# Kernel tuning notes

Hardware: AMD Instinct MI355X
Metric: run time of the kernel (lower is better)

The kernel has to match this reference:

```python
import jax, jax.numpy as jnp
import numpy as np
from jax import lax

T, B = 256, 4096
H = 64  # lstm hidden/input size


def setup_inputs() -> dict:
    key = jax.random.key(0)
    ks = jax.random.split(key, 20)
    s = 0.1
    return {
        "x": jax.random.normal(ks[0], (T * B, 9), jnp.float32),
        "done": jax.random.randint(ks[1], (T * B,), 0, 2).astype(jnp.int32),
        "h0": jax.random.normal(ks[2], (1, B, H), jnp.float32),
        "c0": jax.random.normal(ks[3], (1, B, H), jnp.float32),
        # root MLP: Linear(9,32) ReLU Linear(32,64) ReLU (stored [in,out])
        "Wr1": jax.random.normal(ks[4], (9, 32), jnp.float32) * s,
        "br1": jnp.zeros((32,), jnp.float32),
        "Wr2": jax.random.normal(ks[5], (32, H), jnp.float32) * s,
        "br2": jnp.zeros((H,), jnp.float32),
        # LSTM(64,64): gate order i,f,g,o; stored [in, 4H]
        "Wih": jax.random.normal(ks[6], (H, 4 * H), jnp.float32) * s,
        "Whh": jax.random.normal(ks[7], (H, 4 * H), jnp.float32) * s,
        "b_lstm": jnp.zeros((4 * H,), jnp.float32),  # bias_ih + bias_hh (both init 0)
        # critic: Linear(64,16) Tanh Linear(16,8) Tanh Linear(8,1)
        "Wc1": jax.random.normal(ks[8], (H, 16), jnp.float32) * s,
        "bc1": jnp.zeros((16,), jnp.float32),
        "Wc2": jax.random.normal(ks[9], (16, 8), jnp.float32) * s,
        "bc2": jnp.zeros((8,), jnp.float32),
        "Wc3": jax.random.normal(ks[10], (8, 1), jnp.float32) * s,
        "bc3": jnp.zeros((1,), jnp.float32),
    }


def reference(x, done, h0, c0, Wr1, br1, Wr2, br2, Wih, Whh, b_lstm,
              Wc1, bc1, Wc2, bc2, Wc3, bc3):
    b = h0.shape[1]
    # root MLP on all T*B rows at once
    hidden = jax.nn.relu(jax.nn.relu(x @ Wr1 + br1) @ Wr2 + br2)  # [T*B, 64]
    t = hidden.shape[0] // b
    hid = hidden.reshape(t, b, H)
    d = done.reshape(t, b).astype(hidden.dtype)
    # precompute input projection for all timesteps (hoisted out of the scan)
    xp = hid @ Wih + b_lstm  # [T, B, 4H]

    def step(carry, inp):
        h, c = carry
        xpt, dt = inp
        m = (1.0 - dt)[:, None]  # reset state where episode is done
        h = h * m
        c = c * m
        g = xpt + h @ Whh  # [B, 4H]
        gi, gf, gg, go = jnp.split(g, 4, axis=-1)
        c = jax.nn.sigmoid(gf) * c + jax.nn.sigmoid(gi) * jnp.tanh(gg)
        h = jax.nn.sigmoid(go) * jnp.tanh(c)
        return (h, c), h

    (_, _), hs = lax.scan(step, (h0[0], c0[0]), (xp, d))
    new_hidden = hs.reshape(t * b, H)  # flatten like torch.cat + flatten(0,1)
    # critic head (get_value)
    v = jnp.tanh(new_hidden @ Wc1 + bc1)
    v = jnp.tanh(v @ Wc2 + bc2)
    return v @ Wc3 + bc3  # [T*B, 1]
```

## Files before the change

kernel.cpp:

```cpp
#include <hip/hip_runtime.h>
#include <hip/hip_bf16.h>


#define TT 256
#define BB 4096
#define TBROWS (TT * BB)
#define LOG2E 1.44269504088896340736f

typedef short bf16x8 __attribute__((ext_vector_type(8)));
typedef float f32x4 __attribute__((ext_vector_type(4)));

__device__ __forceinline__ unsigned bfbits(float x) {
  unsigned u = __float_as_uint(x);
  return (u + 0x7fffu + ((u >> 16) & 1u)) >> 16;
}
__device__ __forceinline__ unsigned pkbf(float lo, float hi) {
  return bfbits(lo) | (bfbits(hi) << 16);
}
__device__ __forceinline__ float rcpf_(float x) { return __builtin_amdgcn_rcpf(x); }
__device__ __forceinline__ float exp2f_(float x) { return __builtin_amdgcn_exp2f(x); }

#define BAR_LDS()                                                   \
  do {                                                              \
    asm volatile("s_waitcnt lgkmcnt(0)" ::: "memory");              \
    __builtin_amdgcn_s_barrier();                                   \
    asm volatile("" ::: "memory");                                  \
  } while (0)

__global__ __launch_bounds__(256) void k1m(const float* __restrict__ x,
                                           const float* __restrict__ Wr1,
                                           const float* __restrict__ br1,
                                           const float* __restrict__ Wr2,
                                           const float* __restrict__ br2,
                                           unsigned short* __restrict__ hb) {
  __shared__ int sBr1[2 * 256];
  __shared__ int sBr2[4 * 256];
  __shared__ float sx[4][208];
  __shared__ int h1s[4][324];

  const int tid = threadIdx.x;
  const int lane = tid & 63, wid = tid >> 6;
  const int g4 = lane >> 4, l15 = lane & 15;

  for (int i = tid; i < 512; i += 256) {
    int nt = i >> 8, rem = i & 255;
    int L = rem >> 2, d = rem & 3;
    int u = nt * 16 + (L & 15);
    int k0 = (L >> 4) * 4 + d;
    float v0 = (k0 < 9) ? Wr1[k0 * 32 + u] : 0.f;
    sBr1[i] = (int)bfbits(v0);
  }
  for (int i = tid; i < 1024; i += 256) {
    int nt = i >> 8, rem = i & 255;
    int L = rem >> 2, d = rem & 3;
    int u = nt * 16 + (L & 15);
    int p = (L >> 4) * 4 + d;
    sBr2[i] = (int)pkbf(Wr2[p * 64 + u], Wr2[(p + 16) * 64 + u]);
  }
  __syncthreads();

  float br1v[2] = {br1[l15], br1[16 + l15]};
  float br2v[4];
#pragma unroll
  for (int nt = 0; nt < 4; ++nt) br2v[nt] = br2[nt * 16 + l15];

  long gw = (long)blockIdx.x * 4 + wid;
  long nw = (long)gridDim.x * 4;
  for (long row0 = gw * 16; row0 < TBROWS; row0 += nw * 16) {
    {
      int j = lane;
      float v = x[row0 * 9 + j];
      int r = (j * 456) >> 12; int cc = j - r * 9;
      sx[wid][r * 12 + cc] = v;
      j = lane + 64;
      v = x[row0 * 9 + j];
      r = (j * 456) >> 12; cc = j - r * 9;
      sx[wid][r * 12 + cc] = v;
      if (lane < 16) {
        j = lane + 128;
        v = x[row0 * 9 + j];
        r = (j * 456) >> 12; cc = j - r * 9;
        sx[wid][r * 12 + cc] = v;
      }
    }
    float4 xq = *(const float4*)&sx[wid][l15 * 12 + g4 * 4];
    union { unsigned u[4]; bf16x8 v; } A1;
#pragma unroll
    for (int d = 0; d < 4; ++d) {
      float v = ((const float*)&xq)[d];
      v = (g4 * 4 + d < 9) ? v : 0.f;
      A1.u[d] = bfbits(v);
    }
    f32x4 c1[2];
#pragma unroll
    for (int nt = 0; nt < 2; ++nt) {
      c1[nt] = (f32x4){br1v[nt], br1v[nt], br1v[nt], br1v[nt]};
      c1[nt] = __builtin_amdgcn_mfma_f32_16x16x32_bf16(
          A1.v, *(const bf16x8*)&sBr1[nt * 256 + lane * 4], c1[nt], 0, 0, 0);
    }
#pragma unroll
    for (int r = 0; r < 4; ++r)
      h1s[wid][(g4 * 4 + r) * 20 + l15] =
          (int)pkbf(fmaxf(c1[0][r], 0.f), fmaxf(c1[1][r], 0.f));
    bf16x8 A2 = *(const bf16x8*)&h1s[wid][l15 * 20 + g4 * 4];
    f32x4 c2[4];
#pragma unroll
    for (int nt = 0; nt < 4; ++nt) {
      c2[nt] = (f32x4){br2v[nt], br2v[nt], br2v[nt], br2v[nt]};
      c2[nt] = __builtin_amdgcn_mfma_f32_16x16x32_bf16(
          A2, *(const bf16x8*)&sBr2[nt * 256 + lane * 4], c2[nt], 0, 0, 0);
    }
#pragma unroll
    for (int nt = 0; nt < 4; ++nt)
#pragma unroll
      for (int r = 0; r < 4; ++r)
        hb[(row0 + g4 * 4 + r) * 64 + nt * 16 + l15] =
            (unsigned short)bfbits(fmaxf(c2[nt][r], 0.f));
  }
}

__global__ __launch_bounds__(320) void k2m(
    const unsigned short* __restrict__ hb, const int* __restrict__ done,
    const float* __restrict__ h0, const float* __restrict__ c0,
    const float* __restrict__ Wih, const float* __restrict__ Whh,
    const float* __restrict__ bl,
    const float* __restrict__ Wc1, const float* __restrict__ bc1,
    const float* __restrict__ Wc2, const float* __restrict__ bc2,
    const float* __restrict__ Wc3, const float* __restrict__ bc3,
    float* __restrict__ out) {
  __shared__ __align__(16) unsigned short hT2[2][16 * 72];
  __shared__ float sv1[16 * 20];
  __shared__ int sdone[TT * 16];

  const int tid = threadIdx.x;
  const int lane = tid & 63;
  const int wid = tid >> 6;
  const int g4 = lane >> 4, l15 = lane & 15;
  const int base_b = blockIdx.x * 16;

  for (int i = tid; i < TT * 16; i += 320)
    sdone[i] = done[(long)(i >> 4) * BB + base_b + (i & 15)];

  union frag { unsigned u[4]; bf16x8 v; };
  frag Bih[4][2], Bhh[4][2];
  frag Bc1[2];
  float wc2a[16], wc2b[16];
  float c[4], bias_g[4];
  float bc1s = 0.f, bc2s0 = 0.f, bc2s1 = 0.f, wc3a = 0.f, wc3b = 0.f, bc3r = 0.f;

  if (wid < 4) {
#pragma unroll
    for (int g = 0; g < 4; ++g) {
      int nt = g * 4 + wid;
      int col = nt * 16 + l15;
      float sc = (g == 2) ? 2.f * LOG2E : LOG2E;
#pragma unroll
      for (int q = 0; q < 2; ++q)
#pragma unroll
        for (int d = 0; d < 4; ++d) {
          int k0 = q * 32 + g4 * 8 + 2 * d;
          Bih[g][q].u[d] = pkbf(Wih[k0 * 256 + col] * sc, Wih[(k0 + 1) * 256 + col] * sc);
          Bhh[g][q].u[d] = pkbf(Whh[k0 * 256 + col] * sc, Whh[(k0 + 1) * 256 + col] * sc);
        }
      bias_g[g] = bl[nt * 16 + l15] * sc;
    }
#pragma unroll
    for (int r = 0; r < 4; ++r) {
      int row = base_b + g4 * 4 + r;
      float m0 = 1.f - (float)done[row];
      c[r] = c0[row * 64 + wid * 16 + l15] * m0;
      hT2[1][(g4 * 4 + r) * 72 + wid * 16 + l15] =
          (unsigned short)bfbits(h0[row * 64 + wid * 16 + l15]);
    }
  } else {
    float S = 2.f * LOG2E;
#pragma unroll
    for (int q = 0; q < 2; ++q)
#pragma unroll
      for (int d = 0; d < 4; ++d) {
        int k0 = q * 32 + g4 * 8 + 2 * d;
        Bc1[q].u[d] = pkbf(Wc1[k0 * 16 + l15] * S, Wc1[(k0 + 1) * 16 + l15] * S);
      }
#pragma unroll
    for (int k = 0; k < 16; ++k) {
      wc2a[k] = Wc2[k * 8 + g4 * 2] * S;
      wc2b[k] = Wc2[k * 8 + g4 * 2 + 1] * S;
    }
    bc1s = bc1[l15] * S;
    bc2s0 = bc2[g4 * 2] * S;
    bc2s1 = bc2[g4 * 2 + 1] * S;
    wc3a = Wc3[g4 * 2];
    wc3b = Wc3[g4 * 2 + 1];
    bc3r = bc3[0];
  }
  __syncthreads();

  bf16x8 aA0 = {}, aA1 = {}, aB0 = {}, aB1 = {};
  int dnA = 0, dnB = 0;
  if (wid < 4) {
    long r0a = ((long)0 * BB + base_b + l15) * 64;
    long r1a = ((long)1 * BB + base_b + l15) * 64;
    aA0 = *(const bf16x8*)(hb + r0a + g4 * 8);
    aA1 = *(const bf16x8*)(hb + r0a + 32 + g4 * 8);
    aB0 = *(const bf16x8*)(hb + r1a + g4 * 8);
    aB1 = *(const bf16x8*)(hb + r1a + 32 + g4 * 8);
    dnA = sdone[0 * 16 + l15];
    dnB = sdone[1 * 16 + l15];
  }

  auto gate_step = [&](int t, bf16x8& x0, bf16x8& x1, int& dnv) {
    const unsigned short* rb = hT2[(t + 1) & 1];
    unsigned short* wb = hT2[t & 1];
    int4 r0 = *(const int4*)(rb + l15 * 72 + g4 * 8);
    int4 r1 = *(const int4*)(rb + l15 * 72 + 32 + g4 * 8);
    if (dnv != 0) { r0 = make_int4(0, 0, 0, 0); r1 = make_int4(0, 0, 0, 0); }
    union { int4 i4; bf16x8 v; } ah0, ah1;
    ah0.i4 = r0; ah1.i4 = r1;

    f32x4 accP[4], accQ[4];
#pragma unroll
    for (int g = 0; g < 4; ++g) {
      accP[g] = (f32x4){bias_g[g], bias_g[g], bias_g[g], bias_g[g]};
      accQ[g] = (f32x4){0.f, 0.f, 0.f, 0.f};
    }
#pragma unroll
    for (int g = 0; g < 4; ++g) {
      accP[g] = __builtin_amdgcn_mfma_f32_16x16x32_bf16(ah0.v, Bhh[g][0].v, accP[g], 0, 0, 0);
      accQ[g] = __builtin_amdgcn_mfma_f32_16x16x32_bf16(ah1.v, Bhh[g][1].v, accQ[g], 0, 0, 0);
    }
#pragma unroll
    for (int g = 0; g < 4; ++g) {
      accP[g] = __builtin_amdgcn_mfma_f32_16x16x32_bf16(x0, Bih[g][0].v, accP[g], 0, 0, 0);
      accQ[g] = __builtin_amdgcn_mfma_f32_16x16x32_bf16(x1, Bih[g][1].v, accQ[g], 0, 0, 0);
    }
    if (t + 2 < TT) {
      long nb = ((long)(t + 2) * BB + base_b + l15) * 64;
      x0 = *(const bf16x8*)(hb + nb + g4 * 8);
      x1 = *(const bf16x8*)(hb + nb + 32 + g4 * 8);
      dnv = sdone[(t + 2) * 16 + l15];
    }

    float out_h[4];
#pragma unroll
    for (int r = 0; r < 4; ++r) {
      float xi = accP[0][r] + accQ[0][r];
      float xf = accP[1][r] + accQ[1][r];
      float xg = accP[2][r] + accQ[2][r];
      float xo = accP[3][r] + accQ[3][r];
      float si = rcpf_(1.f + exp2f_(-xi));
      float sf = rcpf_(1.f + exp2f_(-xf));
      float so = rcpf_(1.f + exp2f_(-xo));
      float tg = fmaf(2.f, rcpf_(1.f + exp2f_(-xg)), -1.f);
      float cc = fmaf(sf, c[r], si * tg);
      float tc = fmaf(2.f, rcpf_(1.f + exp2f_(cc * (-2.f * LOG2E))), -1.f);
      out_h[r] = so * tc;
      float mn = (t + 1 < TT) ? (1.f - (float)sdone[(t + 1) * 16 + g4 * 4 + r]) : 1.f;
      c[r] = cc * mn;
    }
#pragma unroll
    for (int r = 0; r < 4; ++r)
      wb[(g4 * 4 + r) * 72 + wid * 16 + l15] = (unsigned short)bfbits(out_h[r]);
  };

  auto critic_step = [&](int tprev, const unsigned short* rb) {
    bf16x8 ca0 = *(const bf16x8*)(rb + l15 * 72 + g4 * 8);
    bf16x8 ca1 = *(const bf16x8*)(rb + l15 * 72 + 32 + g4 * 8);
    f32x4 a1 = (f32x4){bc1s, bc1s, bc1s, bc1s};
    a1 = __builtin_amdgcn_mfma_f32_16x16x32_bf16(ca0, Bc1[0].v, a1, 0, 0, 0);
    a1 = __builtin_amdgcn_mfma_f32_16x16x32_bf16(ca1, Bc1[1].v, a1, 0, 0, 0);
#pragma unroll
    for (int r = 0; r < 4; ++r) {
      float v1 = fmaf(2.f, rcpf_(1.f + exp2f_(-a1[r])), -1.f);
      sv1[(g4 * 4 + r) * 20 + l15] = v1;
    }
    float a2a = bc2s0, a2b = bc2s1;
    const float* vrow = &sv1[l15 * 20];
#pragma unroll
    for (int k = 0; k < 16; ++k) {
      float vk = vrow[k];
      a2a = fmaf(vk, wc2a[k], a2a);
      a2b = fmaf(vk, wc2b[k], a2b);
    }
    float v2a = fmaf(2.f, rcpf_(1.f + exp2f_(-a2a)), -1.f);
    float v2b = fmaf(2.f, rcpf_(1.f + exp2f_(-a2b)), -1.f);
    float p = fmaf(v2a, wc3a, v2b * wc3b);
    p += __shfl_xor(p, 16);
    p += __shfl_xor(p, 32);
    if (g4 == 0) out[(long)tprev * BB + base_b + l15] = p + bc3r;
  };

  for (int t2 = 0; t2 < TT; t2 += 2) {
    if (wid < 4) {
      gate_step(t2, aA0, aA1, dnA);
    } else {
      if (t2 > 0) critic_step(t2 - 1, hT2[(t2 + 1) & 1]);
    }
    BAR_LDS();
    if (wid < 4) {
      gate_step(t2 + 1, aB0, aB1, dnB);
    } else {
      critic_step(t2, hT2[(t2 + 2) & 1]);
    }
    BAR_LDS();
  }
  if (wid == 4) critic_step(TT - 1, hT2[(TT - 1) & 1]);
}

extern "C" void kernel_launch(void* const* d_in, const int* in_sizes, int n_in,
                              void* d_out, int out_size, void* d_ws, size_t ws_size,
                              hipStream_t stream) {
  const float* x = (const float*)d_in[0];
  const int* done = (const int*)d_in[1];
  const float* h0 = (const float*)d_in[2];
  const float* c0 = (const float*)d_in[3];
  const float* Wr1 = (const float*)d_in[4];
  const float* br1 = (const float*)d_in[5];
  const float* Wr2 = (const float*)d_in[6];
  const float* br2 = (const float*)d_in[7];
  const float* Wih = (const float*)d_in[8];
  const float* Whh = (const float*)d_in[9];
  const float* bl = (const float*)d_in[10];
  const float* Wc1 = (const float*)d_in[11];
  const float* bc1 = (const float*)d_in[12];
  const float* Wc2 = (const float*)d_in[13];
  const float* bc2 = (const float*)d_in[14];
  const float* Wc3 = (const float*)d_in[15];
  const float* bc3 = (const float*)d_in[16];
  float* out = (float*)d_out;

  unsigned short* hb = (unsigned short*)d_ws;

  k1m<<<dim3(1024), dim3(256), 0, stream>>>(x, Wr1, br1, Wr2, br2, hb);
  k2m<<<dim3(256), dim3(320), 0, stream>>>(hb, done, h0, c0, Wih, Whh, bl,
                                           Wc1, bc1, Wc2, bc2, Wc3, bc3, out);
}
```

Baseline: 228.5 us.

## Reorder LSTM step MFMAs so input projection overlaps the h load

Inside the recurrent gate step, the input-projection MFMAs (which do not depend on h) now issue before the hidden-state MFMAs. This lets them overlap the LDS read of the previous h, and all four products go into one accumulator per gate, so the P+Q adds disappear. The done-mask is precomputed as floats in shared memory and read with one vector load. bf16 conversion uses the hardware v_cvt_pk_bf16_f32 instruction, and wave priority is raised during the step. This costs extra shared memory for the float mask, and the last step now multiplies c by a real mask instead of 1, which is harmless because c is not used afterwards.

After: 197.5 us. 1.16x faster.

```diff
diff --git a/kernel.cpp b/kernel.cpp
--- a/kernel.cpp
+++ b/kernel.cpp
@@ -16,6 +16,11 @@
 }
 __device__ __forceinline__ unsigned pkbf(float lo, float hi) {
   return bfbits(lo) | (bfbits(hi) << 16);
+}
+__device__ __forceinline__ unsigned short cvt1bf(float x) {
+  unsigned pk;
+  asm("v_cvt_pk_bf16_f32 %0, %1, %2" : "=v"(pk) : "v"(x), "v"(x));
+  return (unsigned short)pk;
 }
 __device__ __forceinline__ float rcpf_(float x) { return __builtin_amdgcn_rcpf(x); }
 __device__ __forceinline__ float exp2f_(float x) { return __builtin_amdgcn_exp2f(x); }
@@ -130,7 +135,8 @@
     float* __restrict__ out) {
   __shared__ __align__(16) unsigned short hT2[2][16 * 72];
   __shared__ float sv1[16 * 20];
-  __shared__ int sdone[TT * 16];
+  __shared__ __align__(16) float smask[TT * 16];
+  __shared__ int sdn[TT * 16];
 
   const int tid = threadIdx.x;
   const int lane = tid & 63;
@@ -138,14 +144,18 @@
   const int g4 = lane >> 4, l15 = lane & 15;
   const int base_b = blockIdx.x * 16;
 
-  for (int i = tid; i < TT * 16; i += 320)
-    sdone[i] = done[(long)(i >> 4) * BB + base_b + (i & 15)];
+  for (int i = tid; i < TT * 16; i += 320) {
+    int d = done[(long)(i >> 4) * BB + base_b + (i & 15)];
+    sdn[i] = d;
+    smask[i] = 1.f - (float)d;
+  }
 
   union frag { unsigned u[4]; bf16x8 v; };
   frag Bih[4][2], Bhh[4][2];
   frag Bc1[2];
   float wc2a[16], wc2b[16];
-  float c[4], bias_g[4];
+  float c[4];
+  f32x4 bias_acc[4];
   float bc1s = 0.f, bc2s0 = 0.f, bc2s1 = 0.f, wc3a = 0.f, wc3b = 0.f, bc3r = 0.f;
 
   if (wid < 4) {
@@ -162,7 +172,8 @@
           Bih[g][q].u[d] = pkbf(Wih[k0 * 256 + col] * sc, Wih[(k0 + 1) * 256 + col] * sc);
           Bhh[g][q].u[d] = pkbf(Whh[k0 * 256 + col] * sc, Whh[(k0 + 1) * 256 + col] * sc);
         }
-      bias_g[g] = bl[nt * 16 + l15] * sc;
+      float bv = bl[nt * 16 + l15] * sc;
+      bias_acc[g] = (f32x4){bv, bv, bv, bv};
     }
 #pragma unroll
     for (int r = 0; r < 4; ++r) {
@@ -204,62 +215,54 @@
     aA1 = *(const bf16x8*)(hb + r0a + 32 + g4 * 8);
     aB0 = *(const bf16x8*)(hb + r1a + g4 * 8);
     aB1 = *(const bf16x8*)(hb + r1a + 32 + g4 * 8);
-    dnA = sdone[0 * 16 + l15];
-    dnB = sdone[1 * 16 + l15];
+    dnA = sdn[0 * 16 + l15];
+    dnB = sdn[1 * 16 + l15];
   }
 
   auto gate_step = [&](int t, bf16x8& x0, bf16x8& x1, int& dnv) {
     const unsigned short* rb = hT2[(t + 1) & 1];
     unsigned short* wb = hT2[t & 1];
+    __builtin_amdgcn_s_setprio(1);
     int4 r0 = *(const int4*)(rb + l15 * 72 + g4 * 8);
     int4 r1 = *(const int4*)(rb + l15 * 72 + 32 + g4 * 8);
+    int tm = (t + 1 < TT) ? t + 1 : t;
+    float4 mn4 = *(const float4*)&smask[tm * 16 + g4 * 4];
+    f32x4 acc[4];
+#pragma unroll
+    for (int g = 0; g < 4; ++g)
+      acc[g] = __builtin_amdgcn_mfma_f32_16x16x32_bf16(x0, Bih[g][0].v, bias_acc[g], 0, 0, 0);
+#pragma unroll
+    for (int g = 0; g < 4; ++g)
+      acc[g] = __builtin_amdgcn_mfma_f32_16x16x32_bf16(x1, Bih[g][1].v, acc[g], 0, 0, 0);
     if (dnv != 0) { r0 = make_int4(0, 0, 0, 0); r1 = make_int4(0, 0, 0, 0); }
     union { int4 i4; bf16x8 v; } ah0, ah1;
     ah0.i4 = r0; ah1.i4 = r1;
-
-    f32x4 accP[4], accQ[4];
-#pragma unroll
-    for (int g = 0; g < 4; ++g) {
-      accP[g] = (f32x4){bias_g[g], bias_g[g], bias_g[g], bias_g[g]};
-      accQ[g] = (f32x4){0.f, 0.f, 0.f, 0.f};
-    }
-#pragma unroll
-    for (int g = 0; g < 4; ++g) {
-      accP[g] = __builtin_amdgcn_mfma_f32_16x16x32_bf16(ah0.v, Bhh[g][0].v, accP[g], 0, 0, 0);
-      accQ[g] = __builtin_amdgcn_mfma_f32_16x16x32_bf16(ah1.v, Bhh[g][1].v, accQ[g], 0, 0, 0);
-    }
-#pragma unroll
-    for (int g = 0; g < 4; ++g) {
-      accP[g] = __builtin_amdgcn_mfma_f32_16x16x32_bf16(x0, Bih[g][0].v, accP[g], 0, 0, 0);
-      accQ[g] = __builtin_amdgcn_mfma_f32_16x16x32_bf16(x1, Bih[g][1].v, accQ[g], 0, 0, 0);
-    }
+#pragma unroll
+    for (int g = 0; g < 4; ++g)
+      acc[g] = __builtin_amdgcn_mfma_f32_16x16x32_bf16(ah0.v, Bhh[g][0].v, acc[g], 0, 0, 0);
+#pragma unroll
+    for (int g = 0; g < 4; ++g)
+      acc[g] = __builtin_amdgcn_mfma_f32_16x16x32_bf16(ah1.v, Bhh[g][1].v, acc[g], 0, 0, 0);
     if (t + 2 < TT) {
       long nb = ((long)(t + 2) * BB + base_b + l15) * 64;
       x0 = *(const bf16x8*)(hb + nb + g4 * 8);
       x1 = *(const bf16x8*)(hb + nb + 32 + g4 * 8);
-      dnv = sdone[(t + 2) * 16 + l15];
-    }
-
-    float out_h[4];
+      dnv = sdn[(t + 2) * 16 + l15];
+    }
 #pragma unroll
     for (int r = 0; r < 4; ++r) {
-      float xi = accP[0][r] + accQ[0][r];
-      float xf = accP[1][r] + accQ[1][r];
-      float xg = accP[2][r] + accQ[2][r];
-      float xo = accP[3][r] + accQ[3][r];
+      float xi = acc[0][r], xf = acc[1][r], xg = acc[2][r], xo = acc[3][r];
       float si = rcpf_(1.f + exp2f_(-xi));
       float sf = rcpf_(1.f + exp2f_(-xf));
       float so = rcpf_(1.f + exp2f_(-xo));
       float tg = fmaf(2.f, rcpf_(1.f + exp2f_(-xg)), -1.f);
       float cc = fmaf(sf, c[r], si * tg);
       float tc = fmaf(2.f, rcpf_(1.f + exp2f_(cc * (-2.f * LOG2E))), -1.f);
-      out_h[r] = so * tc;
-      float mn = (t + 1 < TT) ? (1.f - (float)sdone[(t + 1) * 16 + g4 * 4 + r]) : 1.f;
-      c[r] = cc * mn;
-    }
-#pragma unroll
-    for (int r = 0; r < 4; ++r)
-      wb[(g4 * 4 + r) * 72 + wid * 16 + l15] = (unsigned short)bfbits(out_h[r]);
+      float oh = so * tc;
+      c[r] = cc * ((const float*)&mn4)[r];
+      wb[(g4 * 4 + r) * 72 + wid * 16 + l15] = cvt1bf(oh);
+    }
+    __builtin_amdgcn_s_setprio(0);
   };
 
   auto critic_step = [&](int tprev, const unsigned short* rb) {
```
